# Optimization experiments

Hardware: AMD Instinct MI355X
Metric: run time of the kernel (lower is better)

## Reference

```python
import jax, jax.numpy as jnp
import numpy as np

N_NODES = 100000


def gcn_conv(x, src, dst, W, b, n_nodes):
    """PyG GCNConv: add self-loops, symmetric degree normalization, X W, scatter-add."""
    # Linear transform first (small out dim -> cheaper messages)
    h = x @ W  # [N, F_out]
    # Add self-loops
    loop = jnp.arange(n_nodes, dtype=src.dtype)
    s = jnp.concatenate([src, loop])
    d = jnp.concatenate([dst, loop])
    # Degree (in-degree over dst, incl. self-loops), deg^{-1/2}
    deg = jax.ops.segment_sum(jnp.ones_like(d, dtype=h.dtype), d, num_segments=n_nodes)
    dinv = jnp.where(deg > 0, jax.lax.rsqrt(deg), 0.0)
    norm = dinv[s] * dinv[d]  # [E+N]
    # Gather-scale-scatter aggregation
    msgs = h[s] * norm[:, None]  # [E+N, F_out]
    out = jax.ops.segment_sum(msgs, d, num_segments=n_nodes)
    return out + b


def setup_inputs() -> dict:
    key = jax.random.key(0)
    ks = jax.random.split(key, 4)
    n, f_in, f_hid, f_out = N_NODES, 512, 16, 7
    n_edges = 3200000
    x = jax.random.normal(ks[0], (n, f_in), dtype=jnp.float32)
    edge_index = jax.random.randint(ks[1], (2, n_edges), 0, n, dtype=jnp.int64)
    W1 = jax.random.normal(ks[2], (f_in, f_hid), dtype=jnp.float32) / np.sqrt(f_in)
    b1 = jnp.zeros((f_hid,), dtype=jnp.float32)
    W2 = jax.random.normal(ks[3], (f_hid, f_out), dtype=jnp.float32) / np.sqrt(f_hid)
    b2 = jnp.zeros((f_out,), dtype=jnp.float32)
    return {"x": x, "edge_index": edge_index, "W1": W1, "b1": b1, "W2": W2, "b2": b2}


def reference(x, edge_index, W1, b1, W2, b2):
    n = x.shape[0]
    src, dst = edge_index[0], edge_index[1]
    h = gcn_conv(x, src, dst, W1, b1, n)
    h = jax.nn.relu(h)
    out = gcn_conv(h, src, dst, W2, b2, n)
    return out
```

## Files before the change

### kernel.cpp

```cpp
#include <hip/hip_runtime.h>

#define F_IN 512
#define F_HID 16
#define F_OUT 7
#define BUCKET 128
#define LB 7
#define CHUNK 4096
#define MAXNB 1024
#define BSTR 8192
#define BSTR2 8704

#define KHALF 256
#define WSTR 9

typedef int   int4v   __attribute__((ext_vector_type(4)));
typedef float float2v __attribute__((ext_vector_type(2)));
typedef float float4v __attribute__((ext_vector_type(4)));
typedef unsigned int uint4v __attribute__((ext_vector_type(4)));

static __device__ __forceinline__ unsigned short f2bf(float f) {
    unsigned int u = __float_as_uint(f);
    u += 0x7FFFu + ((u >> 16) & 1u);
    return (unsigned short)(u >> 16);
}
static __device__ __forceinline__ float bf2f(unsigned short s) {
    return __uint_as_float((unsigned int)s << 16);
}

__global__ void k_init(int* __restrict__ cursor, int NB) {
    int i = blockIdx.x * 256 + threadIdx.x;
    if (i < NB) cursor[i] = i * BSTR;
}

__global__ __launch_bounds__(256) void k_place4(
        const int* __restrict__ src, const int* __restrict__ dst,
        int* __restrict__ cursor, int* __restrict__ bedges, int E, int NB) {
    __shared__ int h[MAXNB];
    __shared__ int s[MAXNB];
    __shared__ int sedge[CHUNK];
    __shared__ unsigned short sbkt[CHUNK];
    int t = threadIdx.x, blk = blockIdx.x;
    for (int i = t; i < MAXNB; i += 256) h[i] = 0;
    __syncthreads();
    int base = blk * CHUNK;
    int4v d4[4], s4[4];
#pragma unroll
    for (int it = 0; it < 4; ++it) {
        int e = base + (it * 256 + t) * 4;
        if (e < E) {
            d4[it] = __builtin_nontemporal_load((const int4v*)(dst + e));
            s4[it] = __builtin_nontemporal_load((const int4v*)(src + e));
        } else {
            int sent = NB << LB;
            d4[it].x = sent; d4[it].y = sent; d4[it].z = sent; d4[it].w = sent;
            s4[it].x = 0;    s4[it].y = 0;    s4[it].z = 0;    s4[it].w = 0;
        }
        atomicAdd(&h[d4[it].x >> LB], 1);
        atomicAdd(&h[d4[it].y >> LB], 1);
        atomicAdd(&h[d4[it].z >> LB], 1);
        atomicAdd(&h[d4[it].w >> LB], 1);
    }
    __syncthreads();
    for (int i = t; i < MAXNB; i += 256) s[i] = h[i];
    __syncthreads();
    for (int off = 1; off < MAXNB; off <<= 1) {
        int v[4];
#pragma unroll
        for (int j = 0; j < 4; ++j) {
            int i = t + j * 256;
            v[j] = s[i] + ((i >= off) ? s[i - off] : 0);
        }
        __syncthreads();
#pragma unroll
        for (int j = 0; j < 4; ++j) s[t + j * 256] = v[j];
        __syncthreads();
    }
    for (int i = t; i < MAXNB; i += 256) {
        int incl = s[i], cnt = h[i];
        int excl = incl - cnt;
        h[i] = excl;
        int db = 0;
        if (i < NB && cnt > 0)
            db = atomicAdd(&cursor[i], cnt) - excl;
        s[i] = db;
    }
    __syncthreads();
#pragma unroll
    for (int it = 0; it < 4; ++it) {
        int d, sv, b, p;
        d = d4[it].x; sv = s4[it].x; b = d >> LB; p = atomicAdd(&h[b], 1);
        sedge[p] = (sv << 8) | (d & (BUCKET - 1)); sbkt[p] = (unsigned short)b;
        d = d4[it].y; sv = s4[it].y; b = d >> LB; p = atomicAdd(&h[b], 1);
        sedge[p] = (sv << 8) | (d & (BUCKET - 1)); sbkt[p] = (unsigned short)b;
        d = d4[it].z; sv = s4[it].z; b = d >> LB; p = atomicAdd(&h[b], 1);
        sedge[p] = (sv << 8) | (d & (BUCKET - 1)); sbkt[p] = (unsigned short)b;
        d = d4[it].w; sv = s4[it].w; b = d >> LB; p = atomicAdd(&h[b], 1);
        sedge[p] = (sv << 8) | (d & (BUCKET - 1)); sbkt[p] = (unsigned short)b;
    }
    __syncthreads();
    for (int j = t; j < CHUNK; j += 256) {
        int b = sbkt[j];
        if (b < NB)
            __builtin_nontemporal_store(sedge[j], bedges + s[b] + j);
    }
}

__global__ __launch_bounds__(256) void k_psort(
        const int* __restrict__ cursor, const int* __restrict__ bedges,
        int* __restrict__ bedges2, float* __restrict__ dinv,
        int* __restrict__ node_off, int* __restrict__ node_nq, int n) {
    __shared__ int cnt[BUCKET];
    __shared__ int sc[BUCKET];
    __shared__ int cur[BUCKET];
    __shared__ int sedge[BSTR2];
    int b = blockIdx.x, t = threadIdx.x;
    int base = b * BSTR;
    int ne = cursor[b] - base;
    if (t < BUCKET) cnt[t] = 0;
    __syncthreads();
    int nq = ne >> 2, tail = ne & 3;
    for (int q = t; q < nq; q += 256) {
        int4v v = *(const int4v*)(bedges + base + (q << 2));
        atomicAdd(&cnt[v.x & 127], 1);
        atomicAdd(&cnt[v.y & 127], 1);
        atomicAdd(&cnt[v.z & 127], 1);
        atomicAdd(&cnt[v.w & 127], 1);
    }
    if (t < tail) atomicAdd(&cnt[bedges[base + (nq << 2) + t] & 127], 1);
    __syncthreads();
    int p = 0;
    if (t < BUCKET) { p = (cnt[t] + 3) & ~3; sc[t] = p; }
    __syncthreads();
    for (int off = 1; off < BUCKET; off <<= 1) {
        int v = 0;
        if (t < BUCKET) { v = sc[t]; if (t >= off) v += sc[t - off]; }
        __syncthreads();
        if (t < BUCKET) sc[t] = v;
        __syncthreads();
    }
    if (t < BUCKET) {
        int w = sc[t] - p;
        cur[t] = w;
        int node = b * BUCKET + t;
        if (node < n) {
            dinv[node] = rsqrtf((float)(cnt[t] + 1));
            node_off[node] = b * BSTR2 + w;
            node_nq[node] = p >> 2;
        }
    }
    __syncthreads();
    for (int q = t; q < nq; q += 256) {
        int4v v = *(const int4v*)(bedges + base + (q << 2));
        int pos;
        pos = atomicAdd(&cur[v.x & 127], 1); sedge[pos] = v.x >> 8;
        pos = atomicAdd(&cur[v.y & 127], 1); sedge[pos] = v.y >> 8;
        pos = atomicAdd(&cur[v.z & 127], 1); sedge[pos] = v.z >> 8;
        pos = atomicAdd(&cur[v.w & 127], 1); sedge[pos] = v.w >> 8;
    }
    if (t < tail) {
        int v = bedges[base + (nq << 2) + t];
        int pos = atomicAdd(&cur[v & 127], 1); sedge[pos] = v >> 8;
    }
    __syncthreads();
    if (t < BUCKET) {
        int endc = cur[t];
        for (int i = endc; i < sc[t]; ++i) sedge[i] = n;
    }
    __syncthreads();
    int total = sc[BUCKET - 1];
    int* dst2 = bedges2 + b * BSTR2;
    for (int j4 = t; j4 < (total >> 2); j4 += 256) {
        int4v v = *(const int4v*)(sedge + (j4 << 2));
        __builtin_nontemporal_store(v, (int4v*)(dst2 + (j4 << 2)));
    }
}

__global__ __launch_bounds__(256) void k_gemm1w(
        const float* __restrict__ x, const float* __restrict__ W,
        float* __restrict__ part, int n) {
    __shared__ float2v Ws[256 * WSTR];
    int b  = blockIdx.x >> 1;
    int ks = blockIdx.x & 1;
    int t  = threadIdx.x;
    int kbase = ks * KHALF;

    const float2v* Wg = (const float2v*)(W + (size_t)kbase * F_HID);
#pragma unroll
    for (int it = 0; it < 8; ++it) {
        int m = it * 256 + t;
        Ws[(m >> 3) * WSTR + (m & 7)] = Wg[m];
    }
    __syncthreads();

    int r  = b * 32 + (t >> 3);
    int kl = t & 7;
    if (r < n) {
        const float* xr = x + (size_t)r * F_IN + kbase + kl * 4;
        float4v v[8];
#pragma unroll
        for (int i = 0; i < 8; ++i)
            v[i] = *(const float4v*)(xr + i * 32);

        float2v acc2[8];
#pragma unroll
        for (int c2 = 0; c2 < 8; ++c2) acc2[c2] = (float2v){0.0f, 0.0f};

#pragma unroll
        for (int i = 0; i < 8; ++i) {
            int kb = i * 32 + kl * 4;
#pragma unroll
            for (int j = 0; j < 4; ++j) {
                float xv = v[i][j];
                const float2v* wr = Ws + (kb + j) * WSTR;
#pragma unroll
                for (int c2 = 0; c2 < 8; ++c2)
                    acc2[c2] += xv * wr[c2];
            }
        }
#pragma unroll
        for (int m = 1; m <= 4; m <<= 1) {
#pragma unroll
            for (int c2 = 0; c2 < 8; ++c2) {
                acc2[c2].x += __shfl_xor(acc2[c2].x, m);
                acc2[c2].y += __shfl_xor(acc2[c2].y, m);
            }
        }
        *(float2v*)(part + ((size_t)ks * n + r) * F_HID + kl * 2) = acc2[kl];
    }
}

__global__ void k_fin1(const float* __restrict__ part, const float* __restrict__ dinv,
                       unsigned short* __restrict__ h1b, unsigned short* __restrict__ h2b,
                       int n) {
    int tg = blockIdx.x * 256 + threadIdx.x;
    int r = tg >> 4, c = tg & 15;
    if (r > n) return;
    if (r == n) {
        h1b[(size_t)r * F_HID + c] = 0;
        if (c < 8) h2b[((size_t)r << 3) + c] = 0;
        return;
    }
    float v = part[(size_t)r * F_HID + c] + part[((size_t)n + r) * F_HID + c];
    h1b[(size_t)r * F_HID + c] = f2bf(dinv[r] * v);
}

__global__ __launch_bounds__(1024) void k_aggF1(
        const int* __restrict__ node_off, const int* __restrict__ node_nq,
        const int* __restrict__ bedges2, const unsigned short* __restrict__ h1b,
        const float* __restrict__ dinv, const float* __restrict__ b1,
        const float* __restrict__ W2, unsigned short* __restrict__ h2b, int n) {
    int tg = blockIdx.x * 1024 + threadIdx.x;
    int node = tg >> 4, c = tg & 15;
    if (node >= n) return;
    int off = node_off[node], nq = node_nq[node];
    float acc = bf2f(h1b[(size_t)node * F_HID + c]);
    for (int q = 0; q < nq; ++q) {
        int4v s = *(const int4v*)(bedges2 + off + (q << 2));
        float v0 = bf2f(h1b[(size_t)s.x * F_HID + c]);
        float v1 = bf2f(h1b[(size_t)s.y * F_HID + c]);
        float v2 = bf2f(h1b[(size_t)s.z * F_HID + c]);
        float v3 = bf2f(h1b[(size_t)s.w * F_HID + c]);
        acc += v0 + v1 + v2 + v3;
    }
    float dv = dinv[node];
    float z = fmaxf(dv * acc + b1[c], 0.0f);
    float h[F_OUT];
#pragma unroll
    for (int o = 0; o < F_OUT; ++o) h[o] = z * W2[c * F_OUT + o];
#pragma unroll
    for (int sft = 8; sft >= 1; sft >>= 1)
#pragma unroll
        for (int o = 0; o < F_OUT; ++o) h[o] += __shfl_xor(h[o], sft, 16);
    if (c < 8) {
        unsigned short w = (c < F_OUT) ? f2bf(dv * h[c]) : (unsigned short)0;
        h2b[((size_t)node << 3) + c] = w;
    }
}

__global__ __launch_bounds__(1024) void k_aggF2(
        const int* __restrict__ node_off, const int* __restrict__ node_nq,
        const int* __restrict__ bedges2, const unsigned short* __restrict__ h2b,
        const float* __restrict__ dinv, const float* __restrict__ b2,
        float* __restrict__ out, int n) {
    int tg = blockIdx.x * 1024 + threadIdx.x;
    int node = tg >> 3, c = tg & 7;
    if (node >= n) return;
    int off = node_off[node], nq = node_nq[node];
    float acc = bf2f(h2b[((size_t)node << 3) + c]);
    for (int q = 0; q < nq; ++q) {
        int4v s = *(const int4v*)(bedges2 + off + (q << 2));
        float v0 = bf2f(h2b[((size_t)s.x << 3) + c]);
        float v1 = bf2f(h2b[((size_t)s.y << 3) + c]);
        float v2 = bf2f(h2b[((size_t)s.z << 3) + c]);
        float v3 = bf2f(h2b[((size_t)s.w << 3) + c]);
        acc += v0 + v1 + v2 + v3;
    }
    if (c < F_OUT)
        out[(size_t)node * F_OUT + c] = dinv[node] * acc + b2[c];
}

extern "C" void kernel_launch(void* const* d_in, const int* in_sizes, int n_in,
                              void* d_out, int out_size, void* d_ws, size_t ws_size,
                              hipStream_t stream) {
    const float* x  = (const float*)d_in[0];
    const int*   ei = (const int*)d_in[1];
    const float* W1 = (const float*)d_in[2];
    const float* b1 = (const float*)d_in[3];
    const float* W2 = (const float*)d_in[4];
    const float* b2 = (const float*)d_in[5];
    float* out = (float*)d_out;

    const int n = in_sizes[0] / F_IN;
    const int E = in_sizes[1] / 2;
    const int* src = ei;
    const int* dst = ei + E;

    const int NB = (n + BUCKET - 1) / BUCKET;
    const int PBLK = (E + CHUNK - 1) / CHUNK;
    const int NRB = (n + 31) / 32;

    size_t Np = ((size_t)n + 3) & ~(size_t)3;
    char* ws = (char*)d_ws;
    int*   cursor       = (int*)ws;             ws += MAXNB * 4;
    float* dinv         = (float*)ws;           ws += Np * 4;
    int*   node_off     = (int*)ws;             ws += Np * 4;
    int*   node_nq      = (int*)ws;             ws += Np * 4;
    int*   bedges       = (int*)ws;             ws += (size_t)NB * BSTR * 4;
    int*   bedges2      = (int*)ws;             ws += (size_t)NB * BSTR2 * 4;
    unsigned short* h1b = (unsigned short*)ws;  ws += (Np + 4) * F_HID * 2;
    unsigned short* h2b = (unsigned short*)ws;  ws += (Np + 4) * 8 * 2;
    float* part         = (float*)bedges;

    k_init   <<<(NB + 255) / 256, 256, 0, stream>>>(cursor, NB);
    k_place4 <<<PBLK, 256, 0, stream>>>(src, dst, cursor, bedges, E, NB);
    k_psort  <<<NB, 256, 0, stream>>>(cursor, bedges, bedges2, dinv, node_off, node_nq, n);
    k_gemm1w <<<NRB * 2, 256, 0, stream>>>(x, W1, part, n);
    k_fin1   <<<((n + 1) * 16 + 255) / 256, 256, 0, stream>>>(part, dinv, h1b, h2b, n);
    k_aggF1  <<<((size_t)n * 16 + 1023) / 1024, 1024, 0, stream>>>(node_off, node_nq, bedges2, h1b, dinv, b1, W2, h2b, n);
    k_aggF2  <<<((size_t)n * 8 + 1023) / 1024, 1024, 0, stream>>>(node_off, node_nq, bedges2, h2b, dinv, b2, out, n);
}
```

Baseline: 428.0 us.

## Fuse GEMM finalize into full-K GEMM and pack bf16 pairs in aggregation

The first-layer GEMM now covers the full 512-wide K per block and applies dinv and bf16 conversion itself, so the split-K partial buffer and the separate finalize kernel go away. The zero padding rows for the sentinel node are now written in k_init. Both aggregation kernels read two packed bf16 features per 32-bit load, halving the threads per node and the number of gather instructions. The cost is half as many GEMM blocks, each holding more registers (16 float4 per thread) and more shared memory, which may lower occupancy.

```diff
diff --git a/kernel.cpp b/kernel.cpp
--- a/kernel.cpp
+++ b/kernel.cpp
@@ -10,7 +10,6 @@
 #define BSTR 8192
 #define BSTR2 8704
 
-#define KHALF 256
 #define WSTR 9
 
 typedef int   int4v   __attribute__((ext_vector_type(4)));
@@ -27,9 +26,14 @@
     return __uint_as_float((unsigned int)s << 16);
 }
 
-__global__ void k_init(int* __restrict__ cursor, int NB) {
+__global__ void k_init(int* __restrict__ cursor, unsigned int* __restrict__ h1u,
+                       unsigned int* __restrict__ h2u, int NB, int n) {
     int i = blockIdx.x * 256 + threadIdx.x;
     if (i < NB) cursor[i] = i * BSTR;
+    if (blockIdx.x == 0) {
+        if (threadIdx.x < 8) h1u[(size_t)n * 8 + threadIdx.x] = 0u;
+        if (threadIdx.x < 4) h2u[(size_t)n * 4 + threadIdx.x] = 0u;
+    }
 }
 
 __global__ __launch_bounds__(256) void k_place4(
@@ -175,128 +179,124 @@
     }
 }
 
-__global__ __launch_bounds__(256) void k_gemm1w(
+__global__ __launch_bounds__(256) void k_gemm1wf(
         const float* __restrict__ x, const float* __restrict__ W,
-        float* __restrict__ part, int n) {
-    __shared__ float2v Ws[256 * WSTR];
-    int b  = blockIdx.x >> 1;
-    int ks = blockIdx.x & 1;
-    int t  = threadIdx.x;
-    int kbase = ks * KHALF;
-
-    const float2v* Wg = (const float2v*)(W + (size_t)kbase * F_HID);
-#pragma unroll
-    for (int it = 0; it < 8; ++it) {
+        const float* __restrict__ dinv, unsigned int* __restrict__ h1u, int n) {
+    __shared__ float2v Ws[512 * WSTR];
+    int t = threadIdx.x;
+
+    const float2v* Wg = (const float2v*)W;
+#pragma unroll
+    for (int it = 0; it < 16; ++it) {
         int m = it * 256 + t;
         Ws[(m >> 3) * WSTR + (m & 7)] = Wg[m];
     }
     __syncthreads();
 
-    int r  = b * 32 + (t >> 3);
+    int r  = blockIdx.x * 32 + (t >> 3);
     int kl = t & 7;
-    if (r < n) {
-        const float* xr = x + (size_t)r * F_IN + kbase + kl * 4;
-        float4v v[8];
-#pragma unroll
-        for (int i = 0; i < 8; ++i)
-            v[i] = *(const float4v*)(xr + i * 32);
-
-        float2v acc2[8];
-#pragma unroll
-        for (int c2 = 0; c2 < 8; ++c2) acc2[c2] = (float2v){0.0f, 0.0f};
-
-#pragma unroll
-        for (int i = 0; i < 8; ++i) {
-            int kb = i * 32 + kl * 4;
-#pragma unroll
-            for (int j = 0; j < 4; ++j) {
-                float xv = v[i][j];
-                const float2v* wr = Ws + (kb + j) * WSTR;
-#pragma unroll
-                for (int c2 = 0; c2 < 8; ++c2)
-                    acc2[c2] += xv * wr[c2];
-            }
-        }
-#pragma unroll
-        for (int m = 1; m <= 4; m <<= 1) {
-#pragma unroll
-            for (int c2 = 0; c2 < 8; ++c2) {
-                acc2[c2].x += __shfl_xor(acc2[c2].x, m);
-                acc2[c2].y += __shfl_xor(acc2[c2].y, m);
-            }
-        }
-        *(float2v*)(part + ((size_t)ks * n + r) * F_HID + kl * 2) = acc2[kl];
-    }
-}
-
-__global__ void k_fin1(const float* __restrict__ part, const float* __restrict__ dinv,
-                       unsigned short* __restrict__ h1b, unsigned short* __restrict__ h2b,
-                       int n) {
-    int tg = blockIdx.x * 256 + threadIdx.x;
-    int r = tg >> 4, c = tg & 15;
-    if (r > n) return;
-    if (r == n) {
-        h1b[(size_t)r * F_HID + c] = 0;
-        if (c < 8) h2b[((size_t)r << 3) + c] = 0;
-        return;
-    }
-    float v = part[(size_t)r * F_HID + c] + part[((size_t)n + r) * F_HID + c];
-    h1b[(size_t)r * F_HID + c] = f2bf(dinv[r] * v);
+    if (r >= n) return;
+    const float* xr = x + (size_t)r * F_IN + kl * 4;
+    float4v v[16];
+#pragma unroll
+    for (int i = 0; i < 16; ++i)
+        v[i] = *(const float4v*)(xr + i * 32);
+
+    float2v acc2[8];
+#pragma unroll
+    for (int c2 = 0; c2 < 8; ++c2) acc2[c2] = (float2v){0.0f, 0.0f};
+
+#pragma unroll
+    for (int i = 0; i < 16; ++i) {
+        int kb = i * 32 + kl * 4;
+#pragma unroll
+        for (int j = 0; j < 4; ++j) {
+            float xv = v[i][j];
+            const float2v* wr = Ws + (kb + j) * WSTR;
+#pragma unroll
+            for (int c2 = 0; c2 < 8; ++c2)
+                acc2[c2] += xv * wr[c2];
+        }
+    }
+#pragma unroll
+    for (int m = 1; m <= 4; m <<= 1) {
+#pragma unroll
+        for (int c2 = 0; c2 < 8; ++c2) {
+            acc2[c2].x += __shfl_xor(acc2[c2].x, m);
+            acc2[c2].y += __shfl_xor(acc2[c2].y, m);
+        }
+    }
+    float dv = dinv[r];
+    unsigned int u = (unsigned int)f2bf(dv * acc2[kl].x)
+                   | ((unsigned int)f2bf(dv * acc2[kl].y) << 16);
+    h1u[(size_t)r * 8 + kl] = u;
 }
 
 __global__ __launch_bounds__(1024) void k_aggF1(
         const int* __restrict__ node_off, const int* __restrict__ node_nq,
-        const int* __restrict__ bedges2, const unsigned short* __restrict__ h1b,
+        const int* __restrict__ bedges2, const unsigned int* __restrict__ h1u,
         const float* __restrict__ dinv, const float* __restrict__ b1,
         const float* __restrict__ W2, unsigned short* __restrict__ h2b, int n) {
-    int tg = blockIdx.x * 1024 + threadIdx.x;
-    int node = tg >> 4, c = tg & 15;
-    if (node >= n) return;
-    int off = node_off[node], nq = node_nq[node];
-    float acc = bf2f(h1b[(size_t)node * F_HID + c]);
-    for (int q = 0; q < nq; ++q) {
-        int4v s = *(const int4v*)(bedges2 + off + (q << 2));
-        float v0 = bf2f(h1b[(size_t)s.x * F_HID + c]);
-        float v1 = bf2f(h1b[(size_t)s.y * F_HID + c]);
-        float v2 = bf2f(h1b[(size_t)s.z * F_HID + c]);
-        float v3 = bf2f(h1b[(size_t)s.w * F_HID + c]);
-        acc += v0 + v1 + v2 + v3;
-    }
-    float dv = dinv[node];
-    float z = fmaxf(dv * acc + b1[c], 0.0f);
-    float h[F_OUT];
-#pragma unroll
-    for (int o = 0; o < F_OUT; ++o) h[o] = z * W2[c * F_OUT + o];
-#pragma unroll
-    for (int sft = 8; sft >= 1; sft >>= 1)
-#pragma unroll
-        for (int o = 0; o < F_OUT; ++o) h[o] += __shfl_xor(h[o], sft, 16);
-    if (c < 8) {
-        unsigned short w = (c < F_OUT) ? f2bf(dv * h[c]) : (unsigned short)0;
-        h2b[((size_t)node << 3) + c] = w;
-    }
-}
-
-__global__ __launch_bounds__(1024) void k_aggF2(
-        const int* __restrict__ node_off, const int* __restrict__ node_nq,
-        const int* __restrict__ bedges2, const unsigned short* __restrict__ h2b,
-        const float* __restrict__ dinv, const float* __restrict__ b2,
-        float* __restrict__ out, int n) {
     int tg = blockIdx.x * 1024 + threadIdx.x;
     int node = tg >> 3, c = tg & 7;
     if (node >= n) return;
     int off = node_off[node], nq = node_nq[node];
-    float acc = bf2f(h2b[((size_t)node << 3) + c]);
+    unsigned int su = h1u[(size_t)node * 8 + c];
+    float ax = bf2f((unsigned short)su);
+    float ay = bf2f((unsigned short)(su >> 16));
     for (int q = 0; q < nq; ++q) {
         int4v s = *(const int4v*)(bedges2 + off + (q << 2));
-        float v0 = bf2f(h2b[((size_t)s.x << 3) + c]);
-        float v1 = bf2f(h2b[((size_t)s.y << 3) + c]);
-        float v2 = bf2f(h2b[((size_t)s.z << 3) + c]);
-        float v3 = bf2f(h2b[((size_t)s.w << 3) + c]);
-        acc += v0 + v1 + v2 + v3;
-    }
-    if (c < F_OUT)
-        out[(size_t)node * F_OUT + c] = dinv[node] * acc + b2[c];
+        unsigned int u0 = h1u[(size_t)s.x * 8 + c];
+        unsigned int u1 = h1u[(size_t)s.y * 8 + c];
+        unsigned int u2 = h1u[(size_t)s.z * 8 + c];
+        unsigned int u3 = h1u[(size_t)s.w * 8 + c];
+        ax += bf2f((unsigned short)u0) + bf2f((unsigned short)u1)
+            + bf2f((unsigned short)u2) + bf2f((unsigned short)u3);
+        ay += bf2f((unsigned short)(u0 >> 16)) + bf2f((unsigned short)(u1 >> 16))
+            + bf2f((unsigned short)(u2 >> 16)) + bf2f((unsigned short)(u3 >> 16));
+    }
+    float dv = dinv[node];
+    float zx = fmaxf(dv * ax + b1[2 * c], 0.0f);
+    float zy = fmaxf(dv * ay + b1[2 * c + 1], 0.0f);
+    float h[F_OUT];
+#pragma unroll
+    for (int o = 0; o < F_OUT; ++o)
+        h[o] = zx * W2[(2 * c) * F_OUT + o] + zy * W2[(2 * c + 1) * F_OUT + o];
+#pragma unroll
+    for (int sft = 4; sft >= 1; sft >>= 1)
+#pragma unroll
+        for (int o = 0; o < F_OUT; ++o) h[o] += __shfl_xor(h[o], sft, 8);
+    unsigned short w = (c < F_OUT) ? f2bf(dv * h[c]) : (unsigned short)0;
+    h2b[((size_t)node << 3) + c] = w;
+}
+
+__global__ __launch_bounds__(1024) void k_aggF2(
+        const int* __restrict__ node_off, const int* __restrict__ node_nq,
+        const int* __restrict__ bedges2, const unsigned int* __restrict__ h2u,
+        const float* __restrict__ dinv, const float* __restrict__ b2,
+        float* __restrict__ out, int n) {
+    int tg = blockIdx.x * 1024 + threadIdx.x;
+    int node = tg >> 2, c = tg & 3;
+    if (node >= n) return;
+    int off = node_off[node], nq = node_nq[node];
+    unsigned int su = h2u[(size_t)node * 4 + c];
+    float ax = bf2f((unsigned short)su);
+    float ay = bf2f((unsigned short)(su >> 16));
+    for (int q = 0; q < nq; ++q) {
+        int4v s = *(const int4v*)(bedges2 + off + (q << 2));
+        unsigned int u0 = h2u[(size_t)s.x * 4 + c];
+        unsigned int u1 = h2u[(size_t)s.y * 4 + c];
+        unsigned int u2 = h2u[(size_t)s.z * 4 + c];
+        unsigned int u3 = h2u[(size_t)s.w * 4 + c];
+        ax += bf2f((unsigned short)u0) + bf2f((unsigned short)u1)
+            + bf2f((unsigned short)u2) + bf2f((unsigned short)u3);
+        ay += bf2f((unsigned short)(u0 >> 16)) + bf2f((unsigned short)(u1 >> 16))
+            + bf2f((unsigned short)(u2 >> 16)) + bf2f((unsigned short)(u3 >> 16));
+    }
+    float dv = dinv[node];
+    out[(size_t)node * F_OUT + 2 * c] = dv * ax + b2[2 * c];
+    if (2 * c + 1 < F_OUT)
+        out[(size_t)node * F_OUT + 2 * c + 1] = dv * ay + b2[2 * c + 1];
 }
 
 extern "C" void kernel_launch(void* const* d_in, const int* in_sizes, int n_in,
@@ -329,13 +329,13 @@
     int*   bedges2      = (int*)ws;             ws += (size_t)NB * BSTR2 * 4;
     unsigned short* h1b = (unsigned short*)ws;  ws += (Np + 4) * F_HID * 2;
     unsigned short* h2b = (unsigned short*)ws;  ws += (Np + 4) * 8 * 2;
-    float* part         = (float*)bedges;
-
-    k_init   <<<(NB + 255) / 256, 256, 0, stream>>>(cursor, NB);
-    k_place4 <<<PBLK, 256, 0, stream>>>(src, dst, cursor, bedges, E, NB);
-    k_psort  <<<NB, 256, 0, stream>>>(cursor, bedges, bedges2, dinv, node_off, node_nq, n);
-    k_gemm1w <<<NRB * 2, 256, 0, stream>>>(x, W1, part, n);
-    k_fin1   <<<((n + 1) * 16 + 255) / 256, 256, 0, stream>>>(part, dinv, h1b, h2b, n);
-    k_aggF1  <<<((size_t)n * 16 + 1023) / 1024, 1024, 0, stream>>>(node_off, node_nq, bedges2, h1b, dinv, b1, W2, h2b, n);
-    k_aggF2  <<<((size_t)n * 8 + 1023) / 1024, 1024, 0, stream>>>(node_off, node_nq, bedges2, h2b, dinv, b2, out, n);
-}
+    unsigned int* h1u = (unsigned int*)h1b;
+    unsigned int* h2u = (unsigned int*)h2b;
+
+    k_init    <<<(NB + 255) / 256, 256, 0, stream>>>(cursor, h1u, h2u, NB, n);
+    k_place4  <<<PBLK, 256, 0, stream>>>(src, dst, cursor, bedges, E, NB);
+    k_psort   <<<NB, 256, 0, stream>>>(cursor, bedges, bedges2, dinv, node_off, node_nq, n);
+    k_gemm1wf <<<NRB, 256, 0, stream>>>(x, W1, dinv, h1u, n);
+    k_aggF1   <<<((size_t)n * 8 + 1023) / 1024, 1024, 0, stream>>>(node_off, node_nq, bedges2, h1u, dinv, b1, W2, h2b, n);
+    k_aggF2   <<<((size_t)n * 4 + 1023) / 1024, 1024, 0, stream>>>(node_off, node_nq, bedges2, h2u, dinv, b2, out, n);
+}
```

Measured after the change: 422.2 us. No clear change (-1.4%).
